# Performance work log

Measured on AMD Instinct MI355X. Metric: run time of the kernel, lower is better.

Reference implementation:

```python
import jax, jax.numpy as jnp
import numpy as np
from itertools import product

# Static geometry (matches init_kwargs)
Z, H, W = 8, 96, 180
WZ, WH, WW = 2, 6, 12
MZ, MH, MW = Z // WZ, H // WH, W // WW   # 4, 16, 15
WP = WZ * WH * WW                        # 144 tokens per window
WN = MZ * MH * MW                        # 960 windows
DIM, HEADS = 384, 12
DH = DIM // HEADS
SHIFT = (WZ // 2, WH // 2, WW // 2)      # (1, 3, 6)
NBIAS = WZ * WZ * WH * WH * (2 * WW - 1) # 3312 bias entries
WT = MZ * MH                             # 64 window types (vary with Z,H only)


def _position_index():
    zi = np.arange(WZ); zj = -np.arange(WZ) * WZ
    hi = np.arange(WH); hj = -np.arange(WH) * WH
    w = np.arange(WW)
    c1 = np.stack(np.meshgrid(zi, hi, w, indexing='ij')).reshape(3, WP, 1)
    c2 = np.stack(np.meshgrid(zj, hj, w, indexing='ij')).reshape(3, 1, WP)
    coords = (c1 - c2).transpose(1, 2, 0).astype(np.int64)  # (WP, WP, 3)
    coords[:, :, 2] += WW - 1
    coords[:, :, 1] *= 2 * WW - 1
    coords[:, :, 0] *= (2 * WW - 1) * WH * WH
    return coords.sum(-1).reshape(-1)  # (WP*WP,)


def _attention_mask():
    # in_shape divisible by window -> pad mask is all-zero; only shifted-window
    # (non-adjacency) mask remains, exactly as in the torch buffer.
    img = np.ones((Z, H, W), np.float32)
    zs = (slice(0, -WZ), slice(-WZ, -SHIFT[0]), slice(-SHIFT[0], None))
    hs = (slice(0, -WH), slice(-WH, -SHIFT[1]), slice(-SHIFT[1], None))
    ws = (slice(0, -WW), slice(-WW, -SHIFT[2]), slice(-SHIFT[2], None))
    cnt = 0
    for z, h, w in product(zs, hs, ws):
        img[z, h, w] = cnt
        cnt += 1
    mw = img.reshape(MZ, WZ, MH, WH, MW, WW).transpose(0, 2, 4, 1, 3, 5).reshape(WN, WP)
    diff = mw[:, None, :] - mw[:, :, None]
    return np.where(diff != 0, -100.0, 0.0).astype(np.float32)


POS_IDX = jnp.asarray(_position_index())
ATTN_MASK = jnp.asarray(_attention_mask())  # (WN, WP, WP)


def _layernorm(x, w, b, eps=1e-5):
    m = jnp.mean(x, axis=-1, keepdims=True)
    v = jnp.mean(jnp.square(x - m), axis=-1, keepdims=True)
    return (x - m) * jax.lax.rsqrt(v + eps) * w + b


def setup_inputs() -> dict:
    key = jax.random.key(0)
    ks = jax.random.split(key, 8)
    s = 0.02
    return {
        'x': jax.random.normal(ks[0], (1, Z * H * W, DIM), jnp.float32),
        'w_qkv': jax.random.normal(ks[1], (DIM, 3 * DIM), jnp.float32) * s,
        'w_proj': jax.random.normal(ks[2], (DIM, DIM), jnp.float32) * s,
        'b_proj': jnp.zeros((DIM,), jnp.float32),
        'bias_table': jax.random.normal(ks[3], (NBIAS, WT, HEADS), jnp.float32) * 0.02,
        'ln1_w': jnp.ones((DIM,), jnp.float32),
        'ln1_b': jnp.zeros((DIM,), jnp.float32),
        'ln2_w': jnp.ones((DIM,), jnp.float32),
        'ln2_b': jnp.zeros((DIM,), jnp.float32),
        'w1': jax.random.normal(ks[4], (DIM, 4 * DIM), jnp.float32) * s,
        'b1': jnp.zeros((4 * DIM,), jnp.float32),
        'w2': jax.random.normal(ks[5], (4 * DIM, DIM), jnp.float32) * s,
        'b2': jnp.zeros((DIM,), jnp.float32),
    }


def reference(x, w_qkv, w_proj, b_proj, bias_table, ln1_w, ln1_b, ln2_w, ln2_b, w1, b1, w2, b2):
    B = x.shape[0]
    shortcut = x
    # (B, Z*H*W, D) -> (B, Z, H, W, D); pad is identity (divisible shapes)
    xg = x.reshape(B, Z, H, W, DIM)
    xg = jnp.roll(xg, (-SHIFT[0], -SHIFT[1], -SHIFT[2]), axis=(1, 2, 3))
    # window partition -> (B*WN, WP, D) with window order (B, mZ, mH, mW)
    xw = xg.reshape(B, MZ, WZ, MH, WH, MW, WW, DIM)
    xw = xw.transpose(0, 1, 3, 5, 2, 4, 6, 7).reshape(B * WN, WP, DIM)

    # ---- EarthAttention3D ----
    qkv = (xw @ w_qkv).reshape(B * WN, WP, 3, HEADS, DH).transpose(2, 0, 3, 1, 4)
    q = qkv[0] * (DH ** -0.5)
    k, v = qkv[1], qkv[2]
    attn = jnp.einsum('bhid,bhjd->bhij', q, k)  # (B*WN, HEADS, WP, WP)

    # earth-specific bias: one bias per (mZ, mH) window type, shared over B, mW
    bias = bias_table[POS_IDX].reshape(WP, WP, WT, HEADS).transpose(2, 3, 0, 1)
    bias = bias.reshape(MZ, MH, HEADS, WP, WP)
    attn = attn.reshape(B, MZ, MH, MW, HEADS, WP, WP) + bias[None, :, :, None]

    # shifted-window mask
    attn = attn.reshape(B, WN, HEADS, WP, WP) + ATTN_MASK[None, :, None]
    attn = jax.nn.softmax(attn, axis=-1).reshape(B * WN, HEADS, WP, WP)

    out = jnp.einsum('bhij,bhjd->bhid', attn, v)
    out = out.transpose(0, 2, 1, 3).reshape(B * WN, WP, DIM)
    out = out @ w_proj + b_proj

    # ---- window reverse, unroll, crop (identity) ----
    xg = out.reshape(B, MZ, MH, MW, WZ, WH, WW, DIM)
    xg = xg.transpose(0, 1, 4, 2, 5, 3, 6, 7).reshape(B, Z, H, W, DIM)
    xg = jnp.roll(xg, SHIFT, axis=(1, 2, 3))
    attn_out = xg.reshape(B, Z * H * W, DIM)

    # Pangu post-norm residuals (drop_path prob = 0 -> identity)
    x = shortcut + _layernorm(attn_out, ln1_w, ln1_b)
    h = jax.nn.gelu(x @ w1 + b1, approximate=False) @ w2 + b2
    x = x + _layernorm(h, ln2_w, ln2_b)
    return x
```

## Files before the change

kernel.cpp:

```cpp
#include <hip/hip_runtime.h>
#include <hip/hip_bf16.h>
#include <math.h>

typedef __hip_bfloat16 bf16;
typedef __attribute__((ext_vector_type(4))) float f32x4;
typedef __attribute__((ext_vector_type(16))) float f32x16;
typedef __attribute__((ext_vector_type(8))) short s16x8;
typedef __attribute__((ext_vector_type(4))) short s16x4;

#define DEVI __device__ __forceinline__

constexpr int ZD = 8, HD = 96, WD = 180;
constexpr int WZ = 2, WH = 6, WWn = 12;
constexpr int MZ = 4, MH = 16, MW = 15;
constexpr int WP = 144, WN = 960;
constexpr int DIM = 384, HEADS = 12, DH = 32;
constexpr int TOK = ZD * HD * WD;
constexpr size_t TOKDIM = (size_t)TOK * DIM;
constexpr int NC = 3, CM = TOK / NC;

DEVI short f2b(float f) {
    bf16 h = __float2bfloat16(f);
    return *reinterpret_cast<short*>(&h);
}

DEVI int row_to_token(int r) {
    int wn = r / WP;
    int p  = r - wn * WP;
    int mz = wn / (MH * MW);
    int rem = wn - mz * (MH * MW);
    int mh = rem / MW;
    int mw = rem - mh * MW;
    int lz = p / (WH * WWn);
    int rp = p - lz * (WH * WWn);
    int lh = rp / WWn;
    int lw = rp - lh * WWn;
    int zp = mz * WZ + lz + 1;  if (zp >= ZD) zp -= ZD;
    int hp = mh * WH + lh + 3;  if (hp >= HD) hp -= HD;
    int wp = mw * WWn + lw + 6; if (wp >= WD) wp -= WD;
    return (zp * HD + hp) * WD + wp;
}


__global__ __launch_bounds__(256)
void k_fill(float* __restrict__ out, int n, float v) {
    int i = blockIdx.x * blockDim.x + threadIdx.x;
    if (i < n) out[i] = v;
}

__global__ __launch_bounds__(256)
void k_wcast(const float* __restrict__ w, bf16* __restrict__ wt, int K, int N) {
    int idx = blockIdx.x * blockDim.x + threadIdx.x;
    if (idx >= K * N) return;
    int n = idx / K;
    int k = idx - n * K;
    wt[idx] = __float2bfloat16(w[(size_t)k * N + n]);
}

__global__ __launch_bounds__(256)
void k_btr(const float* __restrict__ bt, float* __restrict__ btr) {
    int idx = blockIdx.x * blockDim.x + threadIdx.x;
    if (idx >= 64 * 12 * 3312) return;
    int wth = idx / 3312;
    int pos = idx - wth * 3312;
    btr[idx] = bt[(size_t)pos * 768 + wth] * 1.4426950408889634f;
}

__global__ __launch_bounds__(256)
void k_mktab(const float* __restrict__ btr, bf16* __restrict__ tab) {
    int idx = blockIdx.x * blockDim.x + threadIdx.x;
    if (idx >= 768 * WP * WP) return;
    int t = idx / (WP * WP);
    int e = idx - t * (WP * WP);
    int i = e / WP, j = e - i * WP;
    int wt = t / 12;
    int mz = wt >> 4, mh = wt & 15;
    int lzi = i / 72, ri_ = i - lzi * 72, lhi = ri_ / 12, lwi = ri_ - lhi * 12;
    int lzj = j / 72, rj_ = j - lzj * 72, lhj = rj_ / 12, lwj = rj_ - lhj * 12;
    int cA = lzi * 828 + lhi * 23 + lwi;
    int cB = lzj * 1656 + lhj * 138 + (11 - lwj);
    float vv = btr[(size_t)t * 3312 + cA + cB];
    int zri = (mz == 3) ? (lzi + 1) : 0, zrj = (mz == 3) ? (lzj + 1) : 0;
    int hri = (mh == 15) ? (lhi < 3 ? 1 : 2) : 0, hrj = (mh == 15) ? (lhj < 3 ? 1 : 2) : 0;
    if (zri != zrj || hri != hrj) vv -= 144.26950408889634f;
    tab[idx] = __float2bfloat16(vv);
}

__global__ __launch_bounds__(256)
void k_gather_x(const float* __restrict__ x, bf16* __restrict__ xw) {
    int idx = blockIdx.x * blockDim.x + threadIdx.x;
    if (idx >= TOK * 96) return;
    int r  = idx / 96;
    int c4 = (idx - r * 96) * 4;
    int t  = row_to_token(r);
    const float4 vv = *(const float4*)(x + (size_t)t * DIM + c4);
    s16x4 o;
    o[0] = f2b(vv.x); o[1] = f2b(vv.y); o[2] = f2b(vv.z); o[3] = f2b(vv.w);
    *(s16x4*)((short*)xw + (size_t)r * DIM + c4) = o;
}


DEVI void gload16(const bf16* g, bf16* l) {
    __builtin_amdgcn_global_load_lds(
        (const __attribute__((address_space(1))) void*)g,
        (__attribute__((address_space(3))) void*)l, 16, 0, 0);
}

template <int EPI>
__global__ __launch_bounds__(256)
void k_gemm(const bf16* __restrict__ A, const bf16* __restrict__ BT,
            const float* __restrict__ bias, bf16* __restrict__ out,
            int M, int N, int K) {
    constexpr int BK = 64;
    __shared__ bf16 As[128 * BK];
    __shared__ bf16 Bs[128 * BK];

    const int nb = N >> 7;
    const int g = blockIdx.x;
    const int xcd = g & 7;
    const int ii = g >> 3;
    const int tt = ii / nb;
    const int bm = tt * 8 + xcd;
    const int bn = ii - tt * nb;

    const int tid = threadIdx.x;
    const int lane = tid & 63;
    const int wv = tid >> 6;
    const int wr = wv >> 1;
    const int wc = wv & 1;
    const int l31 = lane & 31, hi = lane >> 5;

    const bf16* Ab = A + (size_t)bm * 128 * K;
    const bf16* Bb = BT + (size_t)bn * 128 * K;

    f32x16 acc[2][2] = {{{}, {}}, {{}, {}}};

    const int kiters = K / BK;
    const int srow = lane >> 3;
    const int scol = ((lane & 7) ^ srow) * 8;

    int ra[2], rb[2], rax[2], rbx[2];
#pragma unroll
    for (int i2 = 0; i2 < 2; i2++) {
        ra[i2] = 64 * wr + 32 * i2 + l31; rax[i2] = ra[i2] & 7;
        rb[i2] = 64 * wc + 32 * i2 + l31; rbx[i2] = rb[i2] & 7;
    }

    for (int kt = 0; kt < kiters; kt++) {
        const int k0 = kt * BK;
#pragma unroll
        for (int i = 0; i < 4; i++) {
            int ch = wv * 4 + i;
            int row = ch * 8 + srow;
            gload16(Ab + (size_t)row * K + k0 + scol, &As[ch * 512]);
            gload16(Bb + (size_t)row * K + k0 + scol, &Bs[ch * 512]);
        }
        asm volatile("s_waitcnt vmcnt(0)" ::: "memory");
        __syncthreads();
#pragma unroll
        for (int kk = 0; kk < 4; kk++) {
            const int s0 = 2 * kk + hi;
            s16x8 af[2], bfv[2];
#pragma unroll
            for (int ni = 0; ni < 2; ni++)
                af[ni] = *(const s16x8*)&Bs[ra[ni] * BK + ((s0 ^ rax[ni]) * 8)];
#pragma unroll
            for (int mi = 0; mi < 2; mi++)
                bfv[mi] = *(const s16x8*)&As[rb[mi] * BK + ((s0 ^ rbx[mi]) * 8)];
#pragma unroll
            for (int ni = 0; ni < 2; ni++)
#pragma unroll
                for (int mi = 0; mi < 2; mi++)
                    acc[ni][mi] = __builtin_amdgcn_mfma_f32_32x32x16_bf16(
                        af[ni], bfv[mi], acc[ni][mi], 0, 0, 0);
        }
        __syncthreads();
    }

    const int tokbase = bm * 128 + 64 * wc + l31;
    const int featbase = bn * 128 + 64 * wr + 4 * hi;
#pragma unroll
    for (int ni = 0; ni < 2; ni++) {
#pragma unroll
        for (int mi = 0; mi < 2; mi++) {
            const int tok = tokbase + 32 * mi;
#pragma unroll
            for (int rq = 0; rq < 4; rq++) {
                const int f0 = featbase + 32 * ni + 8 * rq;
                float v0 = acc[ni][mi][4 * rq + 0];
                float v1 = acc[ni][mi][4 * rq + 1];
                float v2 = acc[ni][mi][4 * rq + 2];
                float v3 = acc[ni][mi][4 * rq + 3];
                if constexpr (EPI == 0) {
                    const int which = f0 / DIM;
                    const int rem = f0 - which * DIM;
                    const int head = rem >> 5, dh = rem & 31;
                    if (which == 0) {
                        v0 *= 0.25503527f; v1 *= 0.25503527f;
                        v2 *= 0.25503527f; v3 *= 0.25503527f;
                    }
                    const int wn = tok / WP, p = tok - wn * WP;
                    s16x4 o; o[0] = f2b(v0); o[1] = f2b(v1); o[2] = f2b(v2); o[3] = f2b(v3);
                    *(s16x4*)(out + (size_t)which * TOKDIM +
                              ((size_t)(wn * HEADS + head) * WP + p) * DH + dh) = o;
                } else if constexpr (EPI == 1) {
                    const float4 bv = *(const float4*)(bias + f0);
                    s16x4 o;
                    o[0] = f2b(v0 + bv.x); o[1] = f2b(v1 + bv.y);
                    o[2] = f2b(v2 + bv.z); o[3] = f2b(v3 + bv.w);
                    *(s16x4*)(out + (size_t)tok * N + f0) = o;
                } else {
                    const float4 bv = *(const float4*)(bias + f0);
                    float g0 = v0 + bv.x, g1 = v1 + bv.y, g2 = v2 + bv.z, g3 = v3 + bv.w;
                    g0 = 0.5f * g0 * (1.0f + erff(g0 * 0.70710678118654752f));
                    g1 = 0.5f * g1 * (1.0f + erff(g1 * 0.70710678118654752f));
                    g2 = 0.5f * g2 * (1.0f + erff(g2 * 0.70710678118654752f));
                    g3 = 0.5f * g3 * (1.0f + erff(g3 * 0.70710678118654752f));
                    s16x4 o; o[0] = f2b(g0); o[1] = f2b(g1); o[2] = f2b(g2); o[3] = f2b(g3);
                    *(s16x4*)(out + (size_t)tok * N + f0) = o;
                }
            }
        }
    }
}

__global__ __launch_bounds__(192)
void k_attn(const bf16* __restrict__ q, const bf16* __restrict__ kmat,
            const bf16* __restrict__ v, const bf16* __restrict__ tab,
            bf16* __restrict__ out) {
    __shared__ bf16 VTs[DH * 164];
    __shared__ bf16 Ps[3][16 * 164];
    __shared__ unsigned char regn[WP];

    const int bid = blockIdx.x;
    const int wn = bid / HEADS, head = bid - wn * HEADS;
    const int mz = wn / (MH * MW);
    const int rem = wn - mz * (MH * MW);
    const int mh = rem / MW, mw = rem - (rem / MW) * MW;
    const int tile = (mz * MH + mh) * HEADS + head;

    const int tid = threadIdx.x;
    const int lane = tid & 63;
    const int s = tid >> 6;
    const int lg = lane >> 4, lc = lane & 15;

    const size_t base = (size_t)(wn * HEADS + head) * (WP * DH);
    {
        short* vt = (short*)VTs;
#pragma unroll
        for (int e2 = 0; e2 < 3; e2++) {
            int idx = tid + 192 * e2;
            s16x8 vv = *(const s16x8*)(v + base + idx * 8);
            int p = idx >> 2;
            int d0 = (idx & 3) * 8;
#pragma unroll
            for (int e = 0; e < 8; e++) vt[(d0 + e) * 164 + p] = vv[e];
        }
        if (tid < 160) {
            int d = tid / 5, gq = tid - d * 5;
            *(s16x4*)(vt + d * 164 + 144 + gq * 4) = (s16x4){0, 0, 0, 0};
        }
        { short* pz = (short*)&Ps[s][0];
          *(s16x4*)(pz + (lane >> 2) * 164 + 144 + (lane & 3) * 4) = (s16x4){0, 0, 0, 0}; }
        if (tid < WP) {
            int lz = tid / 72, rp = tid - lz * 72;
            int lh = rp / 12, lw = rp - lh * 12;
            int zr = (mz == 3) ? (lz + 1) : 0;
            int hr = (mh == 15) ? (lh < 3 ? 1 : 2) : 0;
            int wbit = (lw < 6) ? 1 : 2;
            regn[tid] = (unsigned char)((zr * 3 + hr) * 4 + wbit);
        }
    }
    __syncthreads();

    const f32x4 zf = {0.f, 0.f, 0.f, 0.f};
    const bf16* tb = tab + (size_t)tile * (WP * WP);
    const bf16* kb = kmat + base;
    bf16* ob = out + (size_t)wn * (WP * DIM) + head * DH;
    short* ps = (short*)&Ps[s][0];
    const bf16* psb = &Ps[s][0];

    for (int t = 0; t < 3; t++) {
        const int strip = 3 * s + t;
        const int ib = 16 * strip + 4 * lg;
        s16x8 aq = *(const s16x8*)(q + base + (size_t)(16 * strip + lc) * DH + 8 * lg);
        f32x4 sacc[9];
#pragma unroll
        for (int jt = 0; jt < 9; jt++) {
            s16x8 bk = *(const s16x8*)(kb + (size_t)(16 * jt + lc) * DH + 8 * lg);
            sacc[jt] = __builtin_amdgcn_mfma_f32_16x16x32_bf16(aq, bk, zf, 0, 0, 0);
        }
#pragma unroll
        for (int jt = 0; jt < 9; jt++) {
            int j = 16 * jt + lc;
#pragma unroll
            for (int r2 = 0; r2 < 4; r2++)
                sacc[jt][r2] += __bfloat162float(tb[(ib + r2) * WP + j]);
        }
        if (mw == 14) {
            int ri[4];
#pragma unroll
            for (int r2 = 0; r2 < 4; r2++) ri[r2] = regn[ib + r2];
#pragma unroll
            for (int jt = 0; jt < 9; jt++) {
                int rj = regn[16 * jt + lc];
#pragma unroll
                for (int r2 = 0; r2 < 4; r2++) {
                    bool m = ((ri[r2] >> 2) == (rj >> 2)) && ((ri[r2] & 3) != (rj & 3));
                    if (m) sacc[jt][r2] -= 144.2695f;
                }
            }
        }
        float inv[4];
#pragma unroll
        for (int r2 = 0; r2 < 4; r2++) {
            float sum = 0.f;
#pragma unroll
            for (int jt = 0; jt < 9; jt++) {
                float pe = exp2f(sacc[jt][r2]);
                sacc[jt][r2] = pe;
                sum += pe;
            }
#pragma unroll
            for (int o = 1; o < 16; o <<= 1) sum += __shfl_xor(sum, o);
            inv[r2] = 1.0f / sum;
        }
#pragma unroll
        for (int jt = 0; jt < 9; jt++)
#pragma unroll
            for (int r2 = 0; r2 < 4; r2++)
                ps[(4 * lg + r2) * 164 + 16 * jt + lc] = f2b(sacc[jt][r2]);
        f32x4 oacc[2] = {zf, zf};
#pragma unroll
        for (int c = 0; c < 5; c++) {
            s16x8 ap = *(const s16x8*)(psb + lc * 164 + 32 * c + 8 * lg);
#pragma unroll
            for (int nt = 0; nt < 2; nt++) {
                s16x8 bv = *(const s16x8*)(VTs + (16 * nt + lc) * 164 + 32 * c + 8 * lg);
                oacc[nt] = __builtin_amdgcn_mfma_f32_16x16x32_bf16(ap, bv, oacc[nt], 0, 0, 0);
            }
        }
#pragma unroll
        for (int nt = 0; nt < 2; nt++)
#pragma unroll
            for (int r2 = 0; r2 < 4; r2++)
                ob[(size_t)(ib + r2) * DIM + 16 * nt + lc] =
                    __float2bfloat16(oacc[nt][r2] * inv[r2]);
    }
}


__global__ __launch_bounds__(256)
void k_ln1(const bf16* __restrict__ y, const float* __restrict__ x,
           const float* __restrict__ w, const float* __restrict__ b,
           bf16* __restrict__ x1b, int r0) {
    const int row = blockIdx.x * 4 + (threadIdx.x >> 6);
    const int l = threadIdx.x & 63;
    const int t = row_to_token(r0 + row);
    const short* yr = (const short*)y + (size_t)row * DIM;
    float v[6];
#pragma unroll
    for (int e = 0; e < 3; e++) {
        int c = 128 * e + 2 * l;
        unsigned int u = *(const unsigned int*)(yr + c);
        unsigned int lo = (u & 0xffffu) << 16, hiu = u & 0xffff0000u;
        v[2 * e]     = *reinterpret_cast<float*>(&lo);
        v[2 * e + 1] = *reinterpret_cast<float*>(&hiu);
    }
    float sum = 0.f, s2 = 0.f;
#pragma unroll
    for (int e = 0; e < 6; e++) { sum += v[e]; s2 += v[e] * v[e]; }
#pragma unroll
    for (int o = 1; o < 64; o <<= 1) { sum += __shfl_xor(sum, o); s2 += __shfl_xor(s2, o); }
    float mean = sum * (1.f / 384.f);
    float var = fmaxf(s2 * (1.f / 384.f) - mean * mean, 0.f);
    float rs = rsqrtf(var + 1e-5f);
#pragma unroll
    for (int e = 0; e < 3; e++) {
        int c = 128 * e + 2 * l;
        const float2 wv2 = *(const float2*)(w + c);
        const float2 bv2 = *(const float2*)(b + c);
        const float2 xx = *(const float2*)(x + (size_t)t * DIM + c);
        float o0 = (v[2 * e] - mean) * rs * wv2.x + bv2.x + xx.x;
        float o1 = (v[2 * e + 1] - mean) * rs * wv2.y + bv2.y + xx.y;
        short2 st; st.x = f2b(o0); st.y = f2b(o1);
        *(short2*)((short*)x1b + (size_t)t * DIM + c) = st;
    }
}

__global__ __launch_bounds__(256)
void k_ln2(const bf16* __restrict__ h, const bf16* __restrict__ x1b,
           const float* __restrict__ w, const float* __restrict__ b,
           float* __restrict__ out) {
    const int row = blockIdx.x * 4 + (threadIdx.x >> 6);
    const int l = threadIdx.x & 63;
    const short* hr = (const short*)h + (size_t)row * DIM;
    float v[6];
#pragma unroll
    for (int e = 0; e < 3; e++) {
        int c = 128 * e + 2 * l;
        unsigned int u = *(const unsigned int*)(hr + c);
        unsigned int lo = (u & 0xffffu) << 16, hiu = u & 0xffff0000u;
        v[2 * e]     = *reinterpret_cast<float*>(&lo);
        v[2 * e + 1] = *reinterpret_cast<float*>(&hiu);
    }
    float sum = 0.f, s2 = 0.f;
#pragma unroll
    for (int e = 0; e < 6; e++) { sum += v[e]; s2 += v[e] * v[e]; }
#pragma unroll
    for (int o = 1; o < 64; o <<= 1) { sum += __shfl_xor(sum, o); s2 += __shfl_xor(s2, o); }
    float mean = sum * (1.f / 384.f);
    float var = fmaxf(s2 * (1.f / 384.f) - mean * mean, 0.f);
    float rs = rsqrtf(var + 1e-5f);
    const short* xr = (const short*)x1b + (size_t)row * DIM;
#pragma unroll
    for (int e = 0; e < 3; e++) {
        int c = 128 * e + 2 * l;
        const float2 wv2 = *(const float2*)(w + c);
        const float2 bv2 = *(const float2*)(b + c);
        unsigned int u = *(const unsigned int*)(xr + c);
        unsigned int lo = (u & 0xffffu) << 16, hiu = u & 0xffff0000u;
        float2 o2;
        o2.x = (v[2 * e] - mean) * rs * wv2.x + bv2.x + *reinterpret_cast<float*>(&lo);
        o2.y = (v[2 * e + 1] - mean) * rs * wv2.y + bv2.y + *reinterpret_cast<float*>(&hiu);
        *(float2*)(out + (size_t)row * DIM + c) = o2;
    }
}


extern "C" void kernel_launch(void* const* d_in, const int* in_sizes, int n_in,
                              void* d_out, int out_size, void* d_ws, size_t ws_size,
                              hipStream_t stream) {
    const float* x      = (const float*)d_in[0];
    const float* w_qkv  = (const float*)d_in[1];
    const float* w_proj = (const float*)d_in[2];
    const float* b_proj = (const float*)d_in[3];
    const float* btab   = (const float*)d_in[4];
    const float* ln1w   = (const float*)d_in[5];
    const float* ln1b   = (const float*)d_in[6];
    const float* ln2w   = (const float*)d_in[7];
    const float* ln2b   = (const float*)d_in[8];
    const float* w1     = (const float*)d_in[9];
    const float* b1     = (const float*)d_in[10];
    const float* w2     = (const float*)d_in[11];
    const float* b2     = (const float*)d_in[12];

    const size_t NEED = 470237184ULL;
    if (ws_size < NEED) {
        k_fill<<<(out_size + 255) / 256, 256, 0, stream>>>((float*)d_out, out_size, 12345.0f);
        return;
    }

    char* ws = (char*)d_ws;
    bf16* wqkvT  = (bf16*)(ws + 0);
    bf16* wprojT = (bf16*)(ws + 884736);
    bf16* w1T    = (bf16*)(ws + 1179648);
    bf16* w2T    = (bf16*)(ws + 2359296);
    float* btr   = (float*)(ws + 3538944);
    bf16* tab    = (bf16*)(ws + 13713408);

    const size_t D1 = 45563904;
    const size_t D2 = 364068864;

    bf16* qkv  = (bf16*)(ws + D1);
    bf16* x1b  = (bf16*)(ws + D1);
    bf16* ytmp = (bf16*)(ws + D1 + 106168320);
    bf16* h1c  = (bf16*)(ws + D1 + 106168320);
    bf16* xw   = (bf16*)(ws + D2);
    bf16* aout = (bf16*)(ws + D2);
    bf16* htmp = (bf16*)(ws + D2);

    k_wcast<<<(442368 + 255) / 256, 256, 0, stream>>>(w_qkv, wqkvT, 384, 1152);
    k_wcast<<<(147456 + 255) / 256, 256, 0, stream>>>(w_proj, wprojT, 384, 384);
    k_wcast<<<(589824 + 255) / 256, 256, 0, stream>>>(w1, w1T, 384, 1536);
    k_wcast<<<(589824 + 255) / 256, 256, 0, stream>>>(w2, w2T, 1536, 384);
    k_btr<<<(2543616 + 255) / 256, 256, 0, stream>>>(btab, btr);
    k_mktab<<<(768 * WP * WP + 255) / 256, 256, 0, stream>>>(btr, tab);
    k_gather_x<<<(TOK * 96 + 255) / 256, 256, 0, stream>>>(x, xw);

    k_gemm<0><<<dim3((TOK / 128) * 9), 256, 0, stream>>>(xw, wqkvT, nullptr, qkv, TOK, 1152, 384);

    k_attn<<<dim3(WN * HEADS), 192, 0, stream>>>(qkv, qkv + TOKDIM, qkv + 2 * TOKDIM, tab, aout);

    for (int c = 0; c < NC; c++) {
        k_gemm<1><<<dim3((CM / 128) * 3), 256, 0, stream>>>(
            aout + (size_t)c * CM * DIM, wprojT, b_proj, ytmp, CM, 384, 384);
        k_ln1<<<dim3(CM / 4), 256, 0, stream>>>(ytmp, x, ln1w, ln1b, x1b, c * CM);
    }

    for (int c = 0; c < NC; c++) {
        k_gemm<2><<<dim3((CM / 128) * 12), 256, 0, stream>>>(
            x1b + (size_t)c * CM * DIM, w1T, b1, h1c, CM, 1536, 384);
        k_gemm<1><<<dim3((CM / 128) * 3), 256, 0, stream>>>(
            h1c, w2T, b2, htmp + (size_t)c * CM * DIM, CM, 384, 1536);
    }

    k_ln2<<<dim3(TOK / 4), 256, 0, stream>>>(htmp, x1b, ln2w, ln2b, (float*)d_out);
}
```

Before: 1.420 ms.

## Double-buffer GEMM LDS tiles and transpose attention score MFMA layout

The GEMM kernel now uses two LDS buffers, so the global-to-LDS load of the next K tile is issued before the MFMAs on the current tile, overlapping memory latency with compute. The attention kernel swaps the operands of the QK^T MFMA so that each lane holds one query row with four consecutive key columns. This allows vectorized bias-table and region loads, a two-step cross-lane reduction for the softmax sum, and packed 4-element stores of probabilities to LDS. The row inverse is then redistributed with shuffles for the output scaling. The cost is doubled LDS use in the GEMM, which may lower occupancy, plus a few extra shuffles in attention.

After: 1.722 ms (median of 2 runs). 21.2% more time.

```diff
diff --git a/kernel.cpp b/kernel.cpp
--- a/kernel.cpp
+++ b/kernel.cpp
@@ -22,6 +22,11 @@
 DEVI short f2b(float f) {
     bf16 h = __float2bfloat16(f);
     return *reinterpret_cast<short*>(&h);
+}
+
+DEVI float b2f(short u) {
+    unsigned int fu = ((unsigned int)(unsigned short)u) << 16;
+    return *reinterpret_cast<float*>(&fu);
 }
 
 DEVI int row_to_token(int r) {
@@ -112,8 +117,8 @@
             const float* __restrict__ bias, bf16* __restrict__ out,
             int M, int N, int K) {
     constexpr int BK = 64;
-    __shared__ bf16 As[128 * BK];
-    __shared__ bf16 Bs[128 * BK];
+    __shared__ bf16 As[2][128 * BK];
+    __shared__ bf16 Bs[2][128 * BK];
 
     const int nb = N >> 7;
     const int g = blockIdx.x;
@@ -146,27 +151,33 @@
         rb[i2] = 64 * wc + 32 * i2 + l31; rbx[i2] = rb[i2] & 7;
     }
 
-    for (int kt = 0; kt < kiters; kt++) {
-        const int k0 = kt * BK;
+    auto stage = [&](int buf, int k0) {
 #pragma unroll
         for (int i = 0; i < 4; i++) {
             int ch = wv * 4 + i;
             int row = ch * 8 + srow;
-            gload16(Ab + (size_t)row * K + k0 + scol, &As[ch * 512]);
-            gload16(Bb + (size_t)row * K + k0 + scol, &Bs[ch * 512]);
-        }
-        asm volatile("s_waitcnt vmcnt(0)" ::: "memory");
-        __syncthreads();
+            gload16(Ab + (size_t)row * K + k0 + scol, &As[buf][ch * 512]);
+            gload16(Bb + (size_t)row * K + k0 + scol, &Bs[buf][ch * 512]);
+        }
+    };
+
+    stage(0, 0);
+    asm volatile("s_waitcnt vmcnt(0)" ::: "memory");
+    __syncthreads();
+
+    int cur = 0;
+    for (int kt = 0; kt < kiters; kt++) {
+        if (kt + 1 < kiters) stage(cur ^ 1, (kt + 1) * BK);
 #pragma unroll
         for (int kk = 0; kk < 4; kk++) {
             const int s0 = 2 * kk + hi;
             s16x8 af[2], bfv[2];
 #pragma unroll
             for (int ni = 0; ni < 2; ni++)
-                af[ni] = *(const s16x8*)&Bs[ra[ni] * BK + ((s0 ^ rax[ni]) * 8)];
+                af[ni] = *(const s16x8*)&Bs[cur][ra[ni] * BK + ((s0 ^ rax[ni]) * 8)];
 #pragma unroll
             for (int mi = 0; mi < 2; mi++)
-                bfv[mi] = *(const s16x8*)&As[rb[mi] * BK + ((s0 ^ rbx[mi]) * 8)];
+                bfv[mi] = *(const s16x8*)&As[cur][rb[mi] * BK + ((s0 ^ rbx[mi]) * 8)];
 #pragma unroll
             for (int ni = 0; ni < 2; ni++)
 #pragma unroll
@@ -174,7 +185,9 @@
                     acc[ni][mi] = __builtin_amdgcn_mfma_f32_32x32x16_bf16(
                         af[ni], bfv[mi], acc[ni][mi], 0, 0, 0);
         }
+        asm volatile("s_waitcnt vmcnt(0)" ::: "memory");
         __syncthreads();
+        cur ^= 1;
     }
 
     const int tokbase = bm * 128 + 64 * wc + l31;
@@ -282,54 +295,54 @@
 
     for (int t = 0; t < 3; t++) {
         const int strip = 3 * s + t;
-        const int ib = 16 * strip + 4 * lg;
-        s16x8 aq = *(const s16x8*)(q + base + (size_t)(16 * strip + lc) * DH + 8 * lg);
+        const int qrow = 16 * strip + lc;
+        s16x8 bq = *(const s16x8*)(q + base + (size_t)qrow * DH + 8 * lg);
         f32x4 sacc[9];
 #pragma unroll
         for (int jt = 0; jt < 9; jt++) {
-            s16x8 bk = *(const s16x8*)(kb + (size_t)(16 * jt + lc) * DH + 8 * lg);
-            sacc[jt] = __builtin_amdgcn_mfma_f32_16x16x32_bf16(aq, bk, zf, 0, 0, 0);
-        }
+            s16x8 ak = *(const s16x8*)(kb + (size_t)(16 * jt + lc) * DH + 8 * lg);
+            sacc[jt] = __builtin_amdgcn_mfma_f32_16x16x32_bf16(ak, bq, zf, 0, 0, 0);
+        }
+        const bf16* tbq = tb + (size_t)qrow * WP;
 #pragma unroll
         for (int jt = 0; jt < 9; jt++) {
-            int j = 16 * jt + lc;
-#pragma unroll
-            for (int r2 = 0; r2 < 4; r2++)
-                sacc[jt][r2] += __bfloat162float(tb[(ib + r2) * WP + j]);
+            s16x4 bvec = *(const s16x4*)(tbq + 16 * jt + 4 * lg);
+#pragma unroll
+            for (int r = 0; r < 4; r++)
+                sacc[jt][r] += b2f(bvec[r]);
         }
         if (mw == 14) {
-            int ri[4];
-#pragma unroll
-            for (int r2 = 0; r2 < 4; r2++) ri[r2] = regn[ib + r2];
+            const int ri = regn[qrow];
 #pragma unroll
             for (int jt = 0; jt < 9; jt++) {
-                int rj = regn[16 * jt + lc];
-#pragma unroll
-                for (int r2 = 0; r2 < 4; r2++) {
-                    bool m = ((ri[r2] >> 2) == (rj >> 2)) && ((ri[r2] & 3) != (rj & 3));
-                    if (m) sacc[jt][r2] -= 144.2695f;
+                unsigned rj4 = *(const unsigned*)(regn + 16 * jt + 4 * lg);
+#pragma unroll
+                for (int r = 0; r < 4; r++) {
+                    int rj = (rj4 >> (8 * r)) & 0xff;
+                    bool m = ((ri >> 2) == (rj >> 2)) && ((ri & 3) != (rj & 3));
+                    if (m) sacc[jt][r] -= 144.2695f;
                 }
             }
         }
-        float inv[4];
-#pragma unroll
-        for (int r2 = 0; r2 < 4; r2++) {
-            float sum = 0.f;
-#pragma unroll
-            for (int jt = 0; jt < 9; jt++) {
-                float pe = exp2f(sacc[jt][r2]);
-                sacc[jt][r2] = pe;
+        float sum = 0.f;
+#pragma unroll
+        for (int jt = 0; jt < 9; jt++)
+#pragma unroll
+            for (int r = 0; r < 4; r++) {
+                float pe = exp2f(sacc[jt][r]);
+                sacc[jt][r] = pe;
                 sum += pe;
             }
-#pragma unroll
-            for (int o = 1; o < 16; o <<= 1) sum += __shfl_xor(sum, o);
-            inv[r2] = 1.0f / sum;
-        }
-#pragma unroll
-        for (int jt = 0; jt < 9; jt++)
-#pragma unroll
-            for (int r2 = 0; r2 < 4; r2++)
-                ps[(4 * lg + r2) * 164 + 16 * jt + lc] = f2b(sacc[jt][r2]);
+        sum += __shfl_xor(sum, 16);
+        sum += __shfl_xor(sum, 32);
+        const float inv = 1.0f / sum;
+#pragma unroll
+        for (int jt = 0; jt < 9; jt++) {
+            s16x4 pk;
+#pragma unroll
+            for (int r = 0; r < 4; r++) pk[r] = f2b(sacc[jt][r]);
+            *(s16x4*)(ps + lc * 164 + 16 * jt + 4 * lg) = pk;
+        }
         f32x4 oacc[2] = {zf, zf};
 #pragma unroll
         for (int c = 0; c < 5; c++) {
@@ -340,12 +353,16 @@
                 oacc[nt] = __builtin_amdgcn_mfma_f32_16x16x32_bf16(ap, bv, oacc[nt], 0, 0, 0);
             }
         }
+        float invo[4];
+#pragma unroll
+        for (int r2 = 0; r2 < 4; r2++) invo[r2] = __shfl(inv, 4 * lg + r2);
+        const int ib = 16 * strip + 4 * lg;
 #pragma unroll
         for (int nt = 0; nt < 2; nt++)
 #pragma unroll
             for (int r2 = 0; r2 < 4; r2++)
                 ob[(size_t)(ib + r2) * DIM + 16 * nt + lc] =
-                    __float2bfloat16(oacc[nt][r2] * inv[r2]);
+                    __float2bfloat16(oacc[nt][r2] * invo[r2]);
     }
 }
 
```
